# Optimization experiments

Measured on AMD Instinct MI355X. Metric: run time of the kernel, lower is better.

Reference implementation:

```python
import jax, jax.numpy as jnp
import numpy as np

BIT = 8          # mantissa bits (incl. sign) shared-exponent BFP
GROUP_SIZE = 16  # elements sharing one exponent


def bfp_quant(x, bit=BIT, group_size=GROUP_SIZE):
    """Block floating-point quantization: flatten, group, share max exponent per group."""
    orig_shape = x.shape
    flat = x.reshape(-1)
    n = flat.shape[0]
    pad = (-n) % group_size
    flat = jnp.pad(flat, (0, pad))
    g = flat.reshape(-1, group_size)                      # [G, group_size]
    m = jnp.max(jnp.abs(g), axis=1, keepdims=True)        # shared magnitude per group
    e = jnp.floor(jnp.log2(jnp.where(m > 0, m, 1.0)))     # shared exponent
    scale = jnp.exp2(e - (bit - 1))                       # quantization step
    qmax = 2.0 ** (bit - 1) - 1
    q = jnp.clip(jnp.round(g / scale), -qmax, qmax) * scale
    q = jnp.where(m > 0, q, 0.0)                          # all-zero groups stay zero
    return q.reshape(-1)[:n].reshape(orig_shape)


def conv2d(x, w, stride=1, padding=1):
    return jax.lax.conv_general_dilated(
        x, w,
        window_strides=(stride, stride),
        padding=((padding, padding), (padding, padding)),
        dimension_numbers=("NCHW", "OIHW", "NCHW"),
    )


def setup_inputs() -> dict:
    key = jax.random.key(0)
    k1, k2 = jax.random.split(key)
    x = jax.random.normal(k1, (64, 128, 56, 56), dtype=jnp.float32)
    fan_in = 128 * 3 * 3
    bound = 1.0 / np.sqrt(fan_in)  # kaiming_uniform_(a=sqrt(5)) -> U(-1/sqrt(fan_in), 1/sqrt(fan_in))
    w = jax.random.uniform(k2, (128, 128, 3, 3), dtype=jnp.float32,
                           minval=-bound, maxval=bound)
    return {"x": x, "w": w}


def reference(x, w):
    # BFConv2dFunction.forward: quantize both operands then conv2d (bias=None, stride=1, padding=1)
    return conv2d(bfp_quant(x), bfp_quant(w), stride=1, padding=1)
```

## Files before the change

kernel.cpp:

```cpp
#include <hip/hip_runtime.h>
#include <hip/hip_bf16.h>


using short8 = __attribute__((ext_vector_type(8))) short;
using f32x4  = __attribute__((ext_vector_type(4))) float;
using int4v  = __attribute__((ext_vector_type(4))) int;

#define XS_STRIDE_S 40
#define XS_ENT      348
#define XS_BUF_S    (XS_ENT * XS_STRIDE_S)

__device__ __forceinline__ unsigned short f2bf(float f) {
    union { float f; unsigned u; } v; v.f = f;
    return (unsigned short)(v.u >> 16);
}

__device__ __forceinline__ void quant16(const float* v, float* o) {
    float m = 0.f;
    #pragma unroll
    for (int i = 0; i < 16; ++i) m = fmaxf(m, fabsf(v[i]));
    if (m > 0.f) {
        float e     = floorf(log2f(m));
        float scale = exp2f(e - 7.0f);
        float inv   = exp2f(7.0f - e);
        #pragma unroll
        for (int i = 0; i < 16; ++i) {
            float q = rintf(v[i] * inv);
            q = fminf(fmaxf(q, -127.f), 127.f);
            o[i] = q * scale;
        }
    } else {
        #pragma unroll
        for (int i = 0; i < 16; ++i) o[i] = 0.f;
    }
}

__global__ __launch_bounds__(256) void quant_kernel(const float* __restrict__ x,
                                                    const float* __restrict__ w,
                                                    unsigned short* __restrict__ xq,
                                                    unsigned short* __restrict__ wq) {
    __shared__ float T[128 * 68];
    const int bid = blockIdx.x;
    const int t   = threadIdx.x;

    if (bid < 3136) {
        const int n  = bid / 49;
        const int p0 = (bid % 49) * 64;
        const float* src = x + (size_t)n * 128 * 3136 + p0;

        #pragma unroll
        for (int i = 0; i < 8; ++i) {
            const int c  = (t >> 4) + i * 16;
            const int ch = t & 15;
            *reinterpret_cast<float4*>(&T[c * 68 + ch * 4]) =
                *reinterpret_cast<const float4*>(src + (size_t)c * 3136 + ch * 4);
        }
        __syncthreads();

        const int c = t & 127;
        #pragma unroll
        for (int i = 0; i < 2; ++i) {
            const int grp = (t >> 7) + 2 * i;
            float v[16];
            #pragma unroll
            for (int j2 = 0; j2 < 4; ++j2) {
                float4 f = *reinterpret_cast<const float4*>(&T[c * 68 + grp * 16 + j2 * 4]);
                v[j2*4+0] = f.x; v[j2*4+1] = f.y; v[j2*4+2] = f.z; v[j2*4+3] = f.w;
            }
            float o[16];
            quant16(v, o);
            unsigned short* dst = xq + ((size_t)(n * 3136 + p0 + grp * 16)) * 128 + c;
            #pragma unroll
            for (int j = 0; j < 16; ++j) dst[(size_t)j * 128] = f2bf(o[j]);
        }
    } else {
        const int G    = (bid - 3136) * 256 + t;
        const int k    = G / 72;
        const int base = (G % 72) * 16;
        const float* src = w + (size_t)k * 1152 + base;
        float v[16];
        #pragma unroll
        for (int i = 0; i < 4; ++i) {
            float4 f = *reinterpret_cast<const float4*>(src + i * 4);
            v[i*4+0] = f.x; v[i*4+1] = f.y; v[i*4+2] = f.z; v[i*4+3] = f.w;
        }
        float o[16];
        quant16(v, o);
        #pragma unroll
        for (int j = 0; j < 16; ++j) {
            int idx2 = base + j;
            int c  = idx2 / 9;
            int rs = idx2 % 9;
            wq[(((size_t)(c >> 5) * 9 + rs) * 128 + k) * 32 + (c & 31)] = f2bf(o[j]);
        }
    }
}

__global__ __launch_bounds__(256, 2) void conv_kernel(const unsigned short* __restrict__ xq,
                                                      const unsigned short* __restrict__ wq,
                                                      float* __restrict__ out) {
    __shared__ __align__(16) unsigned short Xs[2 * XS_BUF_S];

    const int b0   = blockIdx.x;
    const int bid  = (b0 & 7) * 112 + (b0 >> 3);
    const int n    = bid / 14;
    const int h0   = (bid % 14) * 4;
    const int t    = threadIdx.x;
    const int lane = t & 63;
    const int wave = t >> 6;
    const int mw   = wave >> 1;
    const int nw   = wave & 1;

    const unsigned short* sbase[6];
    int  soff[6];
    bool svalid[6], sact[6];
    #pragma unroll
    for (int it = 0; it < 6; ++it) {
        int i   = t + it * 256;
        bool act = i < 1392;
        int e   = i >> 2, cc = i & 3;
        int row = e / 58, pw = e % 58;
        int h   = h0 - 1 + row, w_ = pw - 1;
        bool inb = act && (unsigned)h < 56u && (unsigned)w_ < 56u;
        int gidx = inb ? (n * 3136 + h * 56 + w_) : 0;
        sbase[it]  = xq + (size_t)gidx * 128 + cc * 8;
        soff[it]   = e * XS_STRIDE_S + cc * 8;
        svalid[it] = inb;
        sact[it]   = act;
    }
    int4v sreg[6];

#define STAGE_LOAD(CB) do {                                                    \
    _Pragma("unroll")                                                          \
    for (int it = 0; it < 6; ++it)                                             \
        sreg[it] = svalid[it]                                                  \
            ? *reinterpret_cast<const int4v*>(sbase[it] + (CB) * 32)           \
            : int4v{0, 0, 0, 0};                                               \
} while (0)

#define STAGE_WRITE(BUFS) do {                                                 \
    _Pragma("unroll")                                                          \
    for (int it = 0; it < 6; ++it)                                             \
        if (sact[it])                                                          \
            *reinterpret_cast<int4v*>(Xs + (BUFS) + soff[it]) = sreg[it];      \
} while (0)

    int boff[7];
    #pragma unroll
    for (int fi = 0; fi < 7; ++fi) {
        int m  = mw * 112 + fi * 16 + (lane & 15);
        int dh = m / 56, w_ = m % 56;
        boff[fi] = (dh * 58 + w_) * XS_STRIDE_S + ((lane >> 4) * 8);
    }
    const unsigned short* wk = wq + (size_t)(nw * 64 + (lane & 15)) * 32 + ((lane >> 4) * 8);

#define LOADA(DST, STEP) do {                                                  \
    _Pragma("unroll")                                                          \
    for (int ni = 0; ni < 4; ++ni)                                             \
        DST[ni] = *reinterpret_cast<const short8*>(                            \
            wk + (size_t)(STEP) * 4096 + ni * 512);                            \
} while (0)

    f32x4 acc[7][4];
    #pragma unroll
    for (int fi = 0; fi < 7; ++fi)
        #pragma unroll
        for (int ni = 0; ni < 4; ++ni)
            acc[fi][ni] = f32x4{0.f, 0.f, 0.f, 0.f};

    short8 a_cur[4], a_nxt[4];

    STAGE_LOAD(0);
    LOADA(a_cur, 0);
    STAGE_WRITE(0);
    __syncthreads();

    #pragma unroll
    for (int step = 0; step < 36; ++step) {
        const int cblk = step / 9;
        const int rs   = step % 9;
        const int bufS = (cblk & 1) * XS_BUF_S;

        if (step < 35) LOADA(a_nxt, step + 1);
        if (rs == 0 && cblk < 3) STAGE_LOAD(cblk + 1);

        const int rsS = ((rs / 3) * 58 + (rs % 3)) * XS_STRIDE_S;
        short8 b[7];
        #pragma unroll
        for (int fi = 0; fi < 7; ++fi)
            b[fi] = *reinterpret_cast<const short8*>(Xs + bufS + boff[fi] + rsS);

        #pragma unroll
        for (int fi = 0; fi < 7; ++fi)
            #pragma unroll
            for (int ni = 0; ni < 4; ++ni)
                acc[fi][ni] = __builtin_amdgcn_mfma_f32_16x16x32_bf16(
                    a_cur[ni], b[fi], acc[fi][ni], 0, 0, 0);

        if (rs == 8) {
            if (cblk < 3) STAGE_WRITE(((cblk + 1) & 1) * XS_BUF_S);
            __syncthreads();
        }
        #pragma unroll
        for (int ni = 0; ni < 4; ++ni) a_cur[ni] = a_nxt[ni];
    }

    const int pix0  = h0 * 56 + mw * 112 + (lane & 15);
    const int krow0 = n * 128 + nw * 64 + ((lane >> 4) * 4);
    #pragma unroll
    for (int fi = 0; fi < 7; ++fi)
        #pragma unroll
        for (int ni = 0; ni < 4; ++ni)
            #pragma unroll
            for (int j = 0; j < 4; ++j)
                out[(size_t)(krow0 + ni * 16 + j) * 3136 + pix0 + fi * 16] = acc[fi][ni][j];
#undef LOADA
#undef STAGE_LOAD
#undef STAGE_WRITE
}

extern "C" void kernel_launch(void* const* d_in, const int* in_sizes, int n_in,
                              void* d_out, int out_size, void* d_ws, size_t ws_size,
                              hipStream_t stream) {
    const float* x = (const float*)d_in[0];
    const float* w = (const float*)d_in[1];
    float* out = (float*)d_out;

    unsigned short* xq = (unsigned short*)d_ws;
    unsigned short* wq = xq + (size_t)25690112;

    quant_kernel<<<3136 + 36, 256, 0, stream>>>(x, w, xq, wq);
    conv_kernel <<<896,       256, 0, stream>>>(xq, wq, out);
}
```

Baseline: 257.5 us.

## Stage weight slices into LDS via async global_load_lds with triple buffering

Weights are now streamed into a three-slot LDS ring with global_load_lds instead of being loaded straight into registers per wave, and the weight workspace is re-laid out to match. The activation tile moves from a padded row-stride layout to channel-chunk planes, and its write to LDS is issued earlier in each channel block. Manual vmcnt waits with a barrier every step replace the per-block __syncthreads, and MFMA issue is bracketed with setprio. This aims to cut redundant global weight traffic across waves and overlap loads with MFMA, but adds a barrier on every step and fragile hand-counted waits.

```diff
diff --git a/kernel.cpp b/kernel.cpp
--- a/kernel.cpp
+++ b/kernel.cpp
@@ -6,9 +6,18 @@
 using f32x4  = __attribute__((ext_vector_type(4))) float;
 using int4v  = __attribute__((ext_vector_type(4))) int;
 
-#define XS_STRIDE_S 40
-#define XS_ENT      348
-#define XS_BUF_S    (XS_ENT * XS_STRIDE_S)
+#define XS_PLANE_B 5568
+#define XS_BUF_B   22272
+#define WS_SLICE_B 8192
+#define WS_BASE_B  44544
+
+#define GLL(GSRC, LDST) __builtin_amdgcn_global_load_lds(                      \
+    (const __attribute__((address_space(1))) void*)(GSRC),                     \
+    (__attribute__((address_space(3))) void*)(LDST), 16, 0, 0)
+
+#define WAITV(N) asm volatile("s_waitcnt vmcnt(" #N ")" ::: "memory")
+#define LGKM0()  asm volatile("s_waitcnt lgkmcnt(0)" ::: "memory")
+#define BAR()    asm volatile("s_barrier" ::: "memory")
 
 __device__ __forceinline__ unsigned short f2bf(float f) {
     union { float f; unsigned u; } v; v.f = f;
@@ -47,7 +56,6 @@
         const int n  = bid / 49;
         const int p0 = (bid % 49) * 64;
         const float* src = x + (size_t)n * 128 * 3136 + p0;
-
         #pragma unroll
         for (int i = 0; i < 8; ++i) {
             const int c  = (t >> 4) + i * 16;
@@ -56,7 +64,6 @@
                 *reinterpret_cast<const float4*>(src + (size_t)c * 3136 + ch * 4);
         }
         __syncthreads();
-
         const int c = t & 127;
         #pragma unroll
         for (int i = 0; i < 2; ++i) {
@@ -89,9 +96,11 @@
         #pragma unroll
         for (int j = 0; j < 16; ++j) {
             int idx2 = base + j;
-            int c  = idx2 / 9;
-            int rs = idx2 % 9;
-            wq[(((size_t)(c >> 5) * 9 + rs) * 128 + k) * 32 + (c & 31)] = f2bf(o[j]);
+            int c    = idx2 / 9;
+            int rs   = idx2 % 9;
+            int slice = (c >> 5) * 9 + rs;
+            int c32  = c & 31;
+            wq[(((size_t)slice * 4 + (c32 >> 3)) * 128 + k) * 8 + (c32 & 7)] = f2bf(o[j]);
         }
     }
 }
@@ -99,7 +108,7 @@
 __global__ __launch_bounds__(256, 2) void conv_kernel(const unsigned short* __restrict__ xq,
                                                       const unsigned short* __restrict__ wq,
                                                       float* __restrict__ out) {
-    __shared__ __align__(16) unsigned short Xs[2 * XS_BUF_S];
+    __shared__ __align__(16) char LDSm[WS_BASE_B + 3 * WS_SLICE_B];
 
     const int b0   = blockIdx.x;
     const int bid  = (b0 & 7) * 112 + (b0 >> 3);
@@ -111,6 +120,9 @@
     const int mw   = wave >> 1;
     const int nw   = wave & 1;
 
+    char* XsB = LDSm;
+    char* WsB = LDSm + WS_BASE_B;
+
     const unsigned short* sbase[6];
     int  soff[6];
     bool svalid[6], sact[6];
@@ -124,7 +136,7 @@
         bool inb = act && (unsigned)h < 56u && (unsigned)w_ < 56u;
         int gidx = inb ? (n * 3136 + h * 56 + w_) : 0;
         sbase[it]  = xq + (size_t)gidx * 128 + cc * 8;
-        soff[it]   = e * XS_STRIDE_S + cc * 8;
+        soff[it]   = cc * XS_PLANE_B + e * 16;
         svalid[it] = inb;
         sact[it]   = act;
     }
@@ -134,15 +146,22 @@
     _Pragma("unroll")                                                          \
     for (int it = 0; it < 6; ++it)                                             \
         sreg[it] = svalid[it]                                                  \
-            ? *reinterpret_cast<const int4v*>(sbase[it] + (CB) * 32)           \
+            ? *reinterpret_cast<const int4v*>(sbase[it] + (size_t)(CB) * 32)   \
             : int4v{0, 0, 0, 0};                                               \
 } while (0)
 
-#define STAGE_WRITE(BUFS) do {                                                 \
+#define STAGE_WRITE(BUFB) do {                                                 \
     _Pragma("unroll")                                                          \
     for (int it = 0; it < 6; ++it)                                             \
         if (sact[it])                                                          \
-            *reinterpret_cast<int4v*>(Xs + (BUFS) + soff[it]) = sreg[it];      \
+            *reinterpret_cast<int4v*>(XsB + (BUFB) + soff[it]) = sreg[it];     \
+} while (0)
+
+#define WS_GLL(SLICE) do {                                                     \
+    const unsigned short* gsrc = wq + (size_t)(SLICE) * 4096;                  \
+    char* ldst = WsB + ((SLICE) % 3) * WS_SLICE_B;                             \
+    GLL(gsrc + (size_t)(wave * 128 + lane) * 8,      ldst + wave * 2048);      \
+    GLL(gsrc + (size_t)(wave * 128 + 64 + lane) * 8, ldst + wave * 2048 + 1024);\
 } while (0)
 
     int boff[7];
@@ -150,16 +169,12 @@
     for (int fi = 0; fi < 7; ++fi) {
         int m  = mw * 112 + fi * 16 + (lane & 15);
         int dh = m / 56, w_ = m % 56;
-        boff[fi] = (dh * 58 + w_) * XS_STRIDE_S + ((lane >> 4) * 8);
-    }
-    const unsigned short* wk = wq + (size_t)(nw * 64 + (lane & 15)) * 32 + ((lane >> 4) * 8);
-
-#define LOADA(DST, STEP) do {                                                  \
-    _Pragma("unroll")                                                          \
-    for (int ni = 0; ni < 4; ++ni)                                             \
-        DST[ni] = *reinterpret_cast<const short8*>(                            \
-            wk + (size_t)(STEP) * 4096 + ni * 512);                            \
-} while (0)
+        boff[fi] = (lane >> 4) * XS_PLANE_B + (dh * 58 + w_) * 16;
+    }
+    int aoff[4];
+    #pragma unroll
+    for (int ni = 0; ni < 4; ++ni)
+        aoff[ni] = (lane >> 4) * 2048 + (nw * 64 + ni * 16 + (lane & 15)) * 16;
 
     f32x4 acc[7][4];
     #pragma unroll
@@ -168,41 +183,54 @@
         for (int ni = 0; ni < 4; ++ni)
             acc[fi][ni] = f32x4{0.f, 0.f, 0.f, 0.f};
 
-    short8 a_cur[4], a_nxt[4];
-
+    WS_GLL(0);
+    WS_GLL(1);
     STAGE_LOAD(0);
-    LOADA(a_cur, 0);
+    WAITV(0);
     STAGE_WRITE(0);
-    __syncthreads();
-
-    #pragma unroll
-    for (int step = 0; step < 36; ++step) {
-        const int cblk = step / 9;
-        const int rs   = step % 9;
-        const int bufS = (cblk & 1) * XS_BUF_S;
-
-        if (step < 35) LOADA(a_nxt, step + 1);
+    LGKM0();
+    BAR();
+
+    #pragma unroll
+    for (int s = 0; s < 36; ++s) {
+        const int cblk = s / 9;
+        const int rs   = s % 9;
+        const char* WsS = WsB + (s % 3) * WS_SLICE_B;
+        const char* XsS = XsB + (cblk & 1) * XS_BUF_B;
+        const int rsB   = ((rs / 3) * 58 + (rs % 3)) * 16;
+
+        if (s + 2 < 36) WS_GLL(s + 2);
         if (rs == 0 && cblk < 3) STAGE_LOAD(cblk + 1);
 
-        const int rsS = ((rs / 3) * 58 + (rs % 3)) * XS_STRIDE_S;
-        short8 b[7];
+        short8 a[4], b[7];
+        #pragma unroll
+        for (int ni = 0; ni < 4; ++ni)
+            a[ni] = *reinterpret_cast<const short8*>(WsS + aoff[ni]);
         #pragma unroll
         for (int fi = 0; fi < 7; ++fi)
-            b[fi] = *reinterpret_cast<const short8*>(Xs + bufS + boff[fi] + rsS);
-
+            b[fi] = *reinterpret_cast<const short8*>(XsS + boff[fi] + rsB);
+
+        if (rs == 2 && cblk < 3) {
+            WAITV(4);
+            STAGE_WRITE(((cblk + 1) & 1) * XS_BUF_B);
+        }
+
+        __builtin_amdgcn_s_setprio(1);
         #pragma unroll
         for (int fi = 0; fi < 7; ++fi)
             #pragma unroll
             for (int ni = 0; ni < 4; ++ni)
                 acc[fi][ni] = __builtin_amdgcn_mfma_f32_16x16x32_bf16(
-                    a_cur[ni], b[fi], acc[fi][ni], 0, 0, 0);
-
-        if (rs == 8) {
-            if (cblk < 3) STAGE_WRITE(((cblk + 1) & 1) * XS_BUF_S);
-            __syncthreads();
-        }
-        #pragma unroll
-        for (int ni = 0; ni < 4; ++ni) a_cur[ni] = a_nxt[ni];
+                    a[ni], b[fi], acc[fi][ni], 0, 0, 0);
+        __builtin_amdgcn_s_setprio(0);
+
+        if (s < 35) {
+            if ((rs == 0 || rs == 1) && cblk < 3) WAITV(8);
+            else if (s == 34)                     WAITV(0);
+            else                                  WAITV(2);
+            LGKM0();
+            BAR();
+        }
     }
 
     const int pix0  = h0 * 56 + mw * 112 + (lane & 15);
@@ -214,7 +242,7 @@
             #pragma unroll
             for (int j = 0; j < 4; ++j)
                 out[(size_t)(krow0 + ni * 16 + j) * 3136 + pix0 + fi * 16] = acc[fi][ni][j];
-#undef LOADA
+#undef WS_GLL
 #undef STAGE_LOAD
 #undef STAGE_WRITE
 }
```

Measured after the change: 248.2 us. 1.04x faster.
